# Performance work log

Hardware: AMD Instinct MI355X
Metric: run time of the kernel (lower is better)

## Reference

```python
import jax, jax.numpy as jnp
import numpy as np

B, W, N, K = 8, 16, 40, 10
DN = DL = 128
DE = 128
H = 4
NEG_SLOPE = 0.2


def _build_graph():
    # per-graph ring adjacency: i -> (i+d) % N for d=1..K, in dense_to_sparse order (src-major, dst ascending)
    src0, dst0 = [], []
    for i in range(N):
        ds = sorted(((i + d) % N) for d in range(1, K + 1))
        src0 += [i] * K
        dst0 += ds
    src0 = np.asarray(src0)
    dst0 = np.asarray(dst0)
    G = B * W
    Epg = N * K
    offs = np.arange(G)[:, None] * N
    node_adj = np.stack([(src0[None] + offs).reshape(-1), (dst0[None] + offs).reshape(-1)])
    # line graph: for each node, pair every incoming edge with every outgoing edge (torch repeat/tile order)
    a0, a1, fe = [], [], []
    for num in range(N):
        inc = np.nonzero(dst0 == num)[0]
        out = np.nonzero(src0 == num)[0]
        a0.append(np.repeat(inc, out.size))
        a1.append(np.tile(out, inc.size))
        fe.append(np.full(inc.size * out.size, num))
    a0, a1, fe = np.concatenate(a0), np.concatenate(a1), np.concatenate(fe)
    keep = a0 != a1  # remove_self_loops (no-op here, kept for fidelity)
    a0, a1, fe = a0[keep], a1[keep], fe[keep]
    eoffs = np.arange(G)[:, None] * Epg
    edge_adj = np.stack([(a0[None] + eoffs).reshape(-1), (a1[None] + eoffs).reshape(-1)])
    edge_efea = (fe[None] + offs).reshape(-1)
    return node_adj, edge_adj, edge_efea


def setup_inputs() -> dict:
    key = jax.random.key(0)
    node_adj, edge_adj, edge_efea = _build_graph()
    Epg = N * K
    D1 = DN + DL
    ks = jax.random.split(key, 16)

    def lin(k, fi, fo):
        return jax.random.normal(k, (fi, fo), jnp.float32) / np.sqrt(fi).astype(np.float32)

    return dict(
        x_node=jax.random.normal(ks[0], (B, W, N, DN), jnp.float32),
        x_trace=jax.random.normal(ks[1], (B, W, Epg, DE), jnp.float32),
        x_log=jax.random.normal(ks[2], (B, W, N, DL), jnp.float32),
        node_adj=jnp.asarray(node_adj, jnp.int32),
        edge_adj=jnp.asarray(edge_adj, jnp.int32),
        edge_efea=jnp.asarray(edge_efea, jnp.int32),
        Wl1=lin(ks[3], D1, D1), bl1=jnp.zeros((D1,), jnp.float32),
        Wr1=lin(ks[4], D1, D1), br1=jnp.zeros((D1,), jnp.float32),
        We1=lin(ks[5], DE, D1), be1=jnp.zeros((D1,), jnp.float32),
        att1=jax.random.normal(ks[6], (H, D1 // H), jnp.float32) / np.sqrt(D1 // H).astype(np.float32),
        bias1=jnp.zeros((D1,), jnp.float32),
        Wl2=lin(ks[7], DE, DE), bl2=jnp.zeros((DE,), jnp.float32),
        Wr2=lin(ks[8], DE, DE), br2=jnp.zeros((DE,), jnp.float32),
        We2=lin(ks[9], D1, DE), be2=jnp.zeros((DE,), jnp.float32),
        att2=jax.random.normal(ks[10], (H, DE // H), jnp.float32) / np.sqrt(DE // H).astype(np.float32),
        bias2=jnp.zeros((DE,), jnp.float32),
    )


def _gatv2(x, edge_index, edge_attr, Wl, bl, Wr, br, We, be, att, bias, heads):
    """PyG GATv2Conv (eval mode, add_self_loops=False, concat heads)."""
    n = x.shape[0]
    HC = Wl.shape[1]
    C = HC // heads
    xl = (x @ Wl + bl).reshape(n, heads, C)  # source transform
    xr = (x @ Wr + br).reshape(n, heads, C)  # target transform
    src, dst = edge_index[0], edge_index[1]
    ea = (edge_attr @ We + be).reshape(-1, heads, C)
    m = jax.nn.leaky_relu(xl[src] + xr[dst] + ea, NEG_SLOPE)  # [E,H,C]
    logits = jnp.einsum('ehc,hc->eh', m, att)
    # segment softmax over incoming edges per target node
    mx = jax.ops.segment_max(logits, dst, num_segments=n)
    mx = jnp.where(jnp.isfinite(mx), mx, 0.0)
    ex = jnp.exp(logits - mx[dst])
    den = jax.ops.segment_sum(ex, dst, num_segments=n)
    alpha = ex / (den[dst] + 1e-16)
    out = jax.ops.segment_sum(alpha[:, :, None] * xl[src], dst, num_segments=n)  # [n,H,C]
    return out.reshape(n, HC) + bias


def reference(x_node, x_trace, x_log, node_adj, edge_adj, edge_efea,
              Wl1, bl1, Wr1, br1, We1, be1, att1, bias1,
              Wl2, bl2, Wr2, br2, We2, be2, att2, bias2):
    b, w, n, dn = x_node.shape
    dl = x_log.shape[-1]
    node = jnp.concatenate([x_node, x_log], axis=-1).reshape(-1, dn + dl)  # [G*N, Dn+Dl]
    trace = x_trace.reshape(-1, x_trace.shape[-1])                          # [G*Epg, De]
    node = _gatv2(node, node_adj, trace, Wl1, bl1, Wr1, br1, We1, be1, att1, bias1, H)
    trace = _gatv2(trace, edge_adj, node[edge_efea], Wl2, bl2, Wr2, br2, We2, be2, att2, bias2, H)
    x_node_o = node[:, :dn].reshape(b, w, n, dn)
    x_trace_o = trace.reshape(b, w, -1, trace.shape[-1])
    x_log_o = node[:, dn:].reshape(b, w, n, dl)
    return (x_node_o, x_trace_o, x_log_o)
```

## Files before the change

### kernel.cpp

```cpp
#include <hip/hip_runtime.h>
#include <hip/hip_bf16.h>

#define D1 256
#define DE 128
#define KDEG 10
#define NPG 40
#define EPG 400
#define LOG2E 1.44269504088896340736f

typedef __attribute__((ext_vector_type(8))) short short8;
typedef __attribute__((ext_vector_type(4))) float f32x4;

static inline int cdiv(size_t a, int b) { return (int)((a + b - 1) / b); }
static inline size_t al256(size_t x) { return (x + 255) & ~(size_t)255; }

__device__ __forceinline__ short f2b(float x) {
  __hip_bfloat16 h = __float2bfloat16(x);
  return *reinterpret_cast<short*>(&h);
}

__device__ __forceinline__ short8 cvt8(const float* __restrict__ src) {
  float4 v0 = *(const float4*)src;
  float4 v1 = *(const float4*)(src + 4);
  short8 t;
  t[0] = f2b(v0.x); t[1] = f2b(v0.y); t[2] = f2b(v0.z); t[3] = f2b(v0.w);
  t[4] = f2b(v1.x); t[5] = f2b(v1.y); t[6] = f2b(v1.z); t[7] = f2b(v1.w);
  return t;
}

__global__ __launch_bounds__(256) void k_setup(const float* __restrict__ xn,
                                               const float* __restrict__ xlg,
                                               const float* __restrict__ xtr,
                                               const float* __restrict__ Wl1,
                                               const float* __restrict__ Wr1,
                                               const float* __restrict__ We1,
                                               const float* __restrict__ Wl2,
                                               const float* __restrict__ Wr2,
                                               const float* __restrict__ We2,
                                               const float* __restrict__ bl1,
                                               const float* __restrict__ br1,
                                               const float* __restrict__ be1,
                                               const float* __restrict__ bl2,
                                               const float* __restrict__ br2,
                                               float* __restrict__ den1,
                                               int* __restrict__ cnt,
                                               short* __restrict__ Xb,
                                               short* __restrict__ xtr_b,
                                               short* __restrict__ WT12,
                                               short* __restrict__ WTall,
                                               short* __restrict__ We2T,
                                               float* __restrict__ blr1,
                                               float* __restrict__ bfull,
                                               int NN, int NE) {
  size_t idx = (size_t)blockIdx.x * 256 + threadIdx.x;
  size_t n;
  n = (size_t)NN * 4;       if (idx < n) { den1[idx] = 0.f; return; }           idx -= n;
  n = (size_t)NN;           if (idx < n) { cnt[idx] = 0; return; }              idx -= n;
  n = (size_t)NN * 32;
  if (idx < n) {
    int row = (int)(idx >> 5), q = (int)(idx & 31);
    const float* src = (q < 16) ? &xn[(size_t)row * 128 + q * 8]
                                : &xlg[(size_t)row * 128 + (q - 16) * 8];
    *(short8*)&Xb[(size_t)row * 256 + q * 8] = cvt8(src);
    return;
  }
  idx -= n;
  n = (size_t)NE * 16;
  if (idx < n) {
    *(short8*)&xtr_b[idx * 8] = cvt8(&xtr[idx * 8]);
    return;
  }
  idx -= n;
  n = 512 * 256;
  if (idx < n) {
    int nn = (int)(idx >> 8), k = (int)(idx & 255);
    float v = (nn < 256) ? Wl1[(size_t)k * 256 + nn] : Wr1[(size_t)k * 256 + (nn - 256)];
    WT12[idx] = f2b(v);
    return;
  }
  idx -= n;
  n = 512 * 128;
  if (idx < n) {
    int nn = (int)(idx >> 7), k = (int)(idx & 127);
    float v;
    if (nn < 256)      v = We1[(size_t)k * 256 + nn];
    else if (nn < 384) v = Wl2[(size_t)k * 128 + (nn - 256)];
    else               v = Wr2[(size_t)k * 128 + (nn - 384)];
    WTall[idx] = f2b(v);
    return;
  }
  idx -= n;
  n = 128 * 256;
  if (idx < n) {
    int nn = (int)(idx >> 8), k = (int)(idx & 255);
    We2T[idx] = f2b(We2[(size_t)k * 128 + nn]);
    return;
  }
  idx -= n;
  n = 512;
  if (idx < n) { blr1[idx] = (idx < 256) ? bl1[idx] : br1[idx - 256]; return; }
  idx -= n;
  n = 512;
  if (idx < n) {
    bfull[idx] = (idx < 256) ? be1[idx] : (idx < 384 ? bl2[idx - 256] : br2[idx - 384]);
  }
}

__global__ __launch_bounds__(256) void k_build_inc(const int* __restrict__ adj,
                                                   int* __restrict__ cnt,
                                                   int* __restrict__ inc, int NE) {
  int e = blockIdx.x * 256 + threadIdx.x;
  if (e >= NE) return;
  int dst = adj[NE + e];
  int slot = atomicAdd(&cnt[dst], 1);
  inc[dst * KDEG + slot] = e;
}

__global__ __launch_bounds__(256) void k_gemm_mfma64(const short* __restrict__ A,
                                                     const short* __restrict__ WT,
                                                     const float* __restrict__ bias,
                                                     float* __restrict__ C,
                                                     int M, int K, int N) {
  __shared__ __align__(16) short As[64][40];
  __shared__ __align__(16) short Bs[64][40];
  const int tid = threadIdx.x;
  const int wave = tid >> 6, lane = tid & 63;
  const int quad = lane >> 4, l16 = lane & 15;
  const int m0 = blockIdx.y * 64, n0 = blockIdx.x * 64;
  const int wm = (wave & 1) * 32, wn = (wave >> 1) * 32;
  f32x4 acc[2][2] = {};
  for (int k0 = 0; k0 < K; k0 += 32) {
    {
      int r = tid >> 2, kc = (tid & 3) << 3;
      *(short8*)&As[r][kc] = *(const short8*)&A[(size_t)(m0 + r) * K + (k0 + kc)];
      *(short8*)&Bs[r][kc] = *(const short8*)&WT[(size_t)(n0 + r) * K + (k0 + kc)];
    }
    __syncthreads();
    short8 af[2], bf[2];
    #pragma unroll
    for (int mt = 0; mt < 2; ++mt)
      af[mt] = *(const short8*)&As[wm + mt * 16 + l16][quad << 3];
    #pragma unroll
    for (int nt = 0; nt < 2; ++nt)
      bf[nt] = *(const short8*)&Bs[wn + nt * 16 + l16][quad << 3];
    #pragma unroll
    for (int mt = 0; mt < 2; ++mt)
      #pragma unroll
      for (int nt = 0; nt < 2; ++nt)
        acc[mt][nt] = __builtin_amdgcn_mfma_f32_16x16x32_bf16(
            af[mt], bf[nt], acc[mt][nt], 0, 0, 0);
    __syncthreads();
  }
  #pragma unroll
  for (int nt = 0; nt < 2; ++nt) {
    int col = n0 + wn + nt * 16 + l16;
    float bs = bias[col];
    #pragma unroll
    for (int mt = 0; mt < 2; ++mt) {
      int row = m0 + wm + mt * 16 + (quad << 2);
      #pragma unroll
      for (int r = 0; r < 4; ++r)
        C[(size_t)(row + r) * N + col] = acc[mt][nt][r] + bs;
    }
  }
}

__global__ __launch_bounds__(256) void k_gemm_mega(const short* __restrict__ A,
                                                   const short* __restrict__ WT,
                                                   const float* __restrict__ bfull,
                                                   const float* __restrict__ att1,
                                                   const int* __restrict__ adj,
                                                   const float* __restrict__ xlr1,
                                                   float* __restrict__ logit1,
                                                   float* __restrict__ den1,
                                                   float* __restrict__ pool2,
                                                   int NE) {
  const int K = 128;
  struct SmemGemm { short As[128][40]; short Bs[128][40]; };
  struct SmemEpi  { int sdst[128]; float sxl[14][132]; float sxr[NPG][132]; };
  __shared__ __align__(16) union { SmemGemm g; SmemEpi e; } sm;
  const int tid = threadIdx.x;
  const int wave = tid >> 6, lane = tid & 63;
  const int quad = lane >> 4, l16 = lane & 15;
  int bid = blockIdx.x;
  int l = (bid & 7) * ((int)gridDim.x >> 3) + (bid >> 3);
  const int n0 = (l & 3) << 7;
  const int m0 = (l >> 2) << 7;
  const int wm = (wave & 1) * 64, wn = (wave >> 1) * 64;
  f32x4 acc[4][4] = {};
  for (int k0 = 0; k0 < K; k0 += 32) {
    #pragma unroll
    for (int s = 0; s < 2; ++s) {
      int ch = tid + s * 256;
      int r = ch >> 2, kc = (ch & 3) << 3;
      *(short8*)&sm.g.As[r][kc] = *(const short8*)&A[(size_t)(m0 + r) * K + (k0 + kc)];
      *(short8*)&sm.g.Bs[r][kc] = *(const short8*)&WT[(size_t)(n0 + r) * K + (k0 + kc)];
    }
    __syncthreads();
    short8 af[4], bf[4];
    #pragma unroll
    for (int mt = 0; mt < 4; ++mt)
      af[mt] = *(const short8*)&sm.g.As[wm + mt * 16 + l16][quad << 3];
    #pragma unroll
    for (int nt = 0; nt < 4; ++nt)
      bf[nt] = *(const short8*)&sm.g.Bs[wn + nt * 16 + l16][quad << 3];
    #pragma unroll
    for (int mt = 0; mt < 4; ++mt)
      #pragma unroll
      for (int nt = 0; nt < 4; ++nt)
        acc[mt][nt] = __builtin_amdgcn_mfma_f32_16x16x32_bf16(
            af[mt], bf[nt], acc[mt][nt], 0, 0, 0);
    __syncthreads();
  }
  if (n0 < 256) {
    const int gl = m0 / EPG;
    const int gh = (m0 + 127) / EPG;
    const int slo = m0 / KDEG;
    const int nrl = (m0 + 127) / KDEG - slo + 1;
    if (tid < 128) sm.e.sdst[tid] = adj[NE + m0 + tid];
    for (int s = tid; s < nrl * 128; s += 256) {
      int row = s >> 7, c = s & 127;
      sm.e.sxl[row][c] = xlr1[(size_t)(slo + row) * 512 + n0 + c];
    }
    const int h = (n0 + wn) >> 6;
    float attv[4], bev[4];
    int ccl[4];
    #pragma unroll
    for (int nt = 0; nt < 4; ++nt) {
      int col = n0 + wn + nt * 16 + l16;
      ccl[nt] = col - n0;
      attv[nt] = att1[col] * LOG2E;
      bev[nt] = bfull[col];
    }
    for (int g = gl; g <= gh; ++g) {
      __syncthreads();
      for (int s = tid; s < NPG * 128; s += 256) {
        int row = s >> 7, c = s & 127;
        sm.e.sxr[row][c] = xlr1[(size_t)(g * NPG + row) * 512 + 256 + n0 + c];
      }
      __syncthreads();
      const int elo = g * EPG, ehi = elo + EPG;
      #pragma unroll
      for (int mt = 0; mt < 4; ++mt) {
        #pragma unroll
        for (int r = 0; r < 4; ++r) {
          int le = wm + mt * 16 + (quad << 2) + r;
          int e = m0 + le;
          if (e < elo || e >= ehi) continue;
          int srow = e / KDEG - slo;
          int d = sm.e.sdst[le];
          int drow = d - g * NPG;
          float p = 0.f;
          #pragma unroll
          for (int nt = 0; nt < 4; ++nt) {
            float v = acc[mt][nt][r] + bev[nt] + sm.e.sxl[srow][ccl[nt]]
                    + sm.e.sxr[drow][ccl[nt]];
            v = (v > 0.f) ? v : 0.2f * v;
            p += v * attv[nt];
          }
          p += __shfl_xor(p, 1, 64);
          p += __shfl_xor(p, 2, 64);
          p += __shfl_xor(p, 4, 64);
          p += __shfl_xor(p, 8, 64);
          if (l16 == 0) {
            float ex = exp2f(p);
            logit1[(size_t)e * 4 + h] = ex;
            atomicAdd(&den1[(size_t)d * 4 + h], ex);
          }
        }
      }
    }
  } else {
    #pragma unroll
    for (int nt = 0; nt < 4; ++nt) {
      int col = n0 + wn + nt * 16 + l16;
      float bs = bfull[col];
      int pcol = col - 256;
      #pragma unroll
      for (int mt = 0; mt < 4; ++mt) {
        int row = m0 + wm + mt * 16 + (quad << 2);
        #pragma unroll
        for (int r = 0; r < 4; ++r)
          pool2[(size_t)(row + r) * 256 + pcol] = acc[mt][nt][r] + bs;
      }
    }
  }
}

__global__ __launch_bounds__(256) void k_agg1(const int* __restrict__ adj,
                                              const int* __restrict__ inc,
                                              const float* __restrict__ xlr1,
                                              const float* __restrict__ logit1,
                                              const float* __restrict__ den1,
                                              const float* __restrict__ bias1,
                                              short* __restrict__ nodeoutb,
                                              float* __restrict__ out_node,
                                              float* __restrict__ out_log) {
  int u = blockIdx.x, c = threadIdx.x;
  __shared__ int se[KDEG], ssrc[KDEG];
  __shared__ float slg[KDEG * 4];
  if (c < KDEG) se[c] = inc[u * KDEG + c];
  __syncthreads();
  if (c < KDEG) ssrc[c] = adj[se[c]];
  else if (c >= 64 && c < 64 + KDEG * 4) {
    int t = c - 64;
    slg[t] = logit1[(size_t)se[t >> 2] * 4 + (t & 3)];
  }
  __syncthreads();
  int h = c >> 6;
  float rden = 1.f / (den1[(size_t)u * 4 + h] + 1e-16f);
  float acc = 0.f;
  #pragma unroll
  for (int j = 0; j < KDEG; ++j)
    acc += slg[j * 4 + h] * xlr1[(size_t)ssrc[j] * 512 + c];
  float val = acc * rden + bias1[c];
  nodeoutb[(size_t)u * D1 + c] = f2b(val);
  if (c < 128) out_node[(size_t)u * 128 + c] = val;
  else         out_log[(size_t)u * 128 + (c - 128)] = val;
}

__global__ __launch_bounds__(256) void k_gat2_v4(const int* __restrict__ eadj,
                                                 const int* __restrict__ efea,
                                                 const float* __restrict__ pool2,
                                                 const float* __restrict__ nproj,
                                                 const float* __restrict__ att2,
                                                 const float* __restrict__ bias2,
                                                 float* __restrict__ out_trace,
                                                 int NL) {
  int gi = blockIdx.x;
  size_t le0 = (size_t)gi * 100;
  int t = threadIdx.x;
  __shared__ int ein[KDEG], eout[KDEG], nvs;
  __shared__ float xs[KDEG][132];
  __shared__ float rs[KDEG][132];
  __shared__ float as_[DE];
  __shared__ float exs[400];
  __shared__ float rdn[40];
  if (t < KDEG)          ein[t] = eadj[le0 + (size_t)t * KDEG];
  else if (t < 2 * KDEG) eout[t - KDEG] = eadj[(size_t)NL + le0 + (t - KDEG)];
  else if (t == 255)     nvs = efea[le0];
  __syncthreads();
  int nv = nvs;
  for (int s = t; s < 320; s += 256) {
    int j = s >> 5, q = (s & 31) << 2;
    *(float4*)&xs[j][q] = *(const float4*)&pool2[(size_t)ein[j] * 256 + q];
    float4 tr4 = *(const float4*)&pool2[(size_t)eout[j] * 256 + 128 + q];
    float4 ea4 = *(const float4*)&nproj[(size_t)nv * DE + q];
    float4 r;
    r.x = tr4.x + ea4.x; r.y = tr4.y + ea4.y;
    r.z = tr4.z + ea4.z; r.w = tr4.w + ea4.w;
    *(float4*)&rs[j][q] = r;
  }
  if (t < 32) {
    float4 a4 = *(const float4*)&att2[t << 2];
    float4 o;
    o.x = a4.x * LOG2E; o.y = a4.y * LOG2E;
    o.z = a4.z * LOG2E; o.w = a4.w * LOG2E;
    *(float4*)&as_[t << 2] = o;
  }
  __syncthreads();
  for (int s = t; s < 400; s += 256) {
    int h = s & 3;
    int j = s / 40;
    int o = (s - j * 40) >> 2;
    const float* xa = &xs[j][h << 5];
    const float* ra = &rs[o][h << 5];
    const float* aa = &as_[h << 5];
    float p = 0.f;
    #pragma unroll
    for (int i = 0; i < 32; i += 4) {
      float4 xv = *(const float4*)&xa[i];
      float4 rv = *(const float4*)&ra[i];
      float4 av = *(const float4*)&aa[i];
      float v;
      v = xv.x + rv.x; v = (v > 0.f) ? v : 0.2f * v; p += v * av.x;
      v = xv.y + rv.y; v = (v > 0.f) ? v : 0.2f * v; p += v * av.y;
      v = xv.z + rv.z; v = (v > 0.f) ? v : 0.2f * v; p += v * av.z;
      v = xv.w + rv.w; v = (v > 0.f) ? v : 0.2f * v; p += v * av.w;
    }
    exs[s] = exp2f(p);
  }
  __syncthreads();
  if (t < 40) {
    float d = 0.f;
    #pragma unroll
    for (int j = 0; j < KDEG; ++j) d += exs[(j * 10 + (t >> 2)) * 4 + (t & 3)];
    rdn[t] = 1.f / d;
  }
  __syncthreads();
  {
    int c = t & 127, h = c >> 5, oh = (t >> 7) * 5;
    float bsv = bias2[c];
    #pragma unroll
    for (int oo = 0; oo < 5; ++oo) {
      int o = oh + oo;
      float acc = 0.f;
      #pragma unroll
      for (int j = 0; j < KDEG; ++j)
        acc += exs[(j * 10 + o) * 4 + h] * xs[j][c];
      out_trace[(size_t)eout[o] * DE + c] = acc * rdn[o * 4 + h] + bsv;
    }
  }
}

extern "C" void kernel_launch(void* const* d_in, const int* in_sizes, int n_in,
                              void* d_out, int out_size, void* d_ws, size_t ws_size,
                              hipStream_t stream) {
  const float* x_node   = (const float*)d_in[0];
  const float* x_trace  = (const float*)d_in[1];
  const float* x_log    = (const float*)d_in[2];
  const int*   node_adj = (const int*)d_in[3];
  const int*   edge_adj = (const int*)d_in[4];
  const int*   edge_efea= (const int*)d_in[5];
  const float* Wl1 = (const float*)d_in[6];
  const float* bl1 = (const float*)d_in[7];
  const float* Wr1 = (const float*)d_in[8];
  const float* br1 = (const float*)d_in[9];
  const float* We1 = (const float*)d_in[10];
  const float* be1 = (const float*)d_in[11];
  const float* att1 = (const float*)d_in[12];
  const float* bias1 = (const float*)d_in[13];
  const float* Wl2 = (const float*)d_in[14];
  const float* bl2 = (const float*)d_in[15];
  const float* Wr2 = (const float*)d_in[16];
  const float* br2 = (const float*)d_in[17];
  const float* We2 = (const float*)d_in[18];
  const float* be2 = (const float*)d_in[19];
  const float* att2 = (const float*)d_in[20];
  const float* bias2 = (const float*)d_in[21];

  const int NN = in_sizes[0] / 128;
  const int NE = in_sizes[1] / 128;
  const int NL = in_sizes[5];

  char* p = (char*)d_ws;
  float* pool2   = (float*)p; p += al256((size_t)NE * 256 * 4);
  float* xlr1    = (float*)p; p += al256((size_t)NN * 512 * 4);
  short* Xb      = (short*)p; p += al256((size_t)NN * D1 * 2);
  short* xtr_b   = (short*)p; p += al256((size_t)NE * DE * 2);
  short* nodeoutb= (short*)p; p += al256((size_t)NN * D1 * 2);
  float* nproj   = (float*)p; p += al256((size_t)NN * DE * 4);
  float* logit1  = (float*)p; p += al256((size_t)NE * 4 * 4);
  float* den1    = (float*)p; p += al256((size_t)NN * 4 * 4);
  int*   inc     = (int*)p;   p += al256((size_t)NN * KDEG * 4);
  int*   cnt     = (int*)p;   p += al256((size_t)NN * 4);
  short* WT12    = (short*)p; p += al256((size_t)512 * 256 * 2);
  short* WTall   = (short*)p; p += al256((size_t)512 * 128 * 2);
  short* We2T    = (short*)p; p += al256((size_t)128 * 256 * 2);
  float* blr1    = (float*)p; p += al256(512 * 4);
  float* bfull   = (float*)p; p += al256(512 * 4);
  (void)ws_size;

  float* out_node  = (float*)d_out;
  float* out_trace = out_node + (size_t)NN * 128;
  float* out_log   = out_trace + (size_t)NE * 128;

  {
    size_t total = (size_t)NN * 5 + (size_t)NN * 32 + (size_t)NE * 16 +
                   512 * 256 + 512 * 128 + 128 * 256 + 512 + 512;
    k_setup<<<cdiv(total, 256), 256, 0, stream>>>(x_node, x_log, x_trace,
                                                  Wl1, Wr1, We1, Wl2, Wr2, We2,
                                                  bl1, br1, be1, bl2, br2,
                                                  den1, cnt, Xb, xtr_b,
                                                  WT12, WTall, We2T, blr1, bfull,
                                                  NN, NE);
  }
  k_build_inc<<<cdiv(NE, 256), 256, 0, stream>>>(node_adj, cnt, inc, NE);

  k_gemm_mfma64<<<dim3(512 / 64, NN / 64), 256, 0, stream>>>(Xb, WT12, blr1, xlr1,
                                                             NN, D1, 512);

  k_gemm_mega<<<4 * (NE / 128), 256, 0, stream>>>(xtr_b, WTall, bfull, att1,
                                                  node_adj, xlr1, logit1, den1,
                                                  pool2, NE);

  k_agg1<<<NN, 256, 0, stream>>>(node_adj, inc, xlr1, logit1, den1, bias1,
                                 nodeoutb, out_node, out_log);

  k_gemm_mfma64<<<dim3(DE / 64, NN / 64), 256, 0, stream>>>(nodeoutb, We2T, be2,
                                                            nproj, NN, D1, DE);
  k_gat2_v4<<<NN, 256, 0, stream>>>(edge_adj, edge_efea, pool2, nproj,
                                    att2, bias2, out_trace, NL);
}
```

Before: 236.9 us.

## Fuse layer-2 edge projections into GAT2 kernel, drop pool2 intermediate

```diff
diff --git a/kernel.cpp b/kernel.cpp
--- a/kernel.cpp
+++ b/kernel.cpp
@@ -6,6 +6,7 @@
 #define KDEG 10
 #define NPG 40
 #define EPG 400
+#define GNODES 2
 #define LOG2E 1.44269504088896340736f
 
 typedef __attribute__((ext_vector_type(8))) short short8;
@@ -173,7 +174,6 @@
                                                    const float* __restrict__ xlr1,
                                                    float* __restrict__ logit1,
                                                    float* __restrict__ den1,
-                                                   float* __restrict__ pool2,
                                                    int NE) {
   const int K = 128;
   struct SmemGemm { short As[128][40]; short Bs[128][40]; };
@@ -184,8 +184,8 @@
   const int quad = lane >> 4, l16 = lane & 15;
   int bid = blockIdx.x;
   int l = (bid & 7) * ((int)gridDim.x >> 3) + (bid >> 3);
-  const int n0 = (l & 3) << 7;
-  const int m0 = (l >> 2) << 7;
+  const int n0 = (l & 1) << 7;
+  const int m0 = (l >> 1) << 7;
   const int wm = (wave & 1) * 64, wn = (wave >> 1) * 64;
   f32x4 acc[4][4] = {};
   for (int k0 = 0; k0 < K; k0 += 32) {
@@ -212,76 +212,60 @@
             af[mt], bf[nt], acc[mt][nt], 0, 0, 0);
     __syncthreads();
   }
-  if (n0 < 256) {
-    const int gl = m0 / EPG;
-    const int gh = (m0 + 127) / EPG;
-    const int slo = m0 / KDEG;
-    const int nrl = (m0 + 127) / KDEG - slo + 1;
-    if (tid < 128) sm.e.sdst[tid] = adj[NE + m0 + tid];
-    for (int s = tid; s < nrl * 128; s += 256) {
+  const int gl = m0 / EPG;
+  const int gh = (m0 + 127) / EPG;
+  const int slo = m0 / KDEG;
+  const int nrl = (m0 + 127) / KDEG - slo + 1;
+  if (tid < 128) sm.e.sdst[tid] = adj[NE + m0 + tid];
+  for (int s = tid; s < nrl * 128; s += 256) {
+    int row = s >> 7, c = s & 127;
+    sm.e.sxl[row][c] = xlr1[(size_t)(slo + row) * 512 + n0 + c];
+  }
+  const int h = (n0 + wn) >> 6;
+  float attv[4], bev[4];
+  int ccl[4];
+  #pragma unroll
+  for (int nt = 0; nt < 4; ++nt) {
+    int col = n0 + wn + nt * 16 + l16;
+    ccl[nt] = col - n0;
+    attv[nt] = att1[col] * LOG2E;
+    bev[nt] = bfull[col];
+  }
+  for (int g = gl; g <= gh; ++g) {
+    __syncthreads();
+    for (int s = tid; s < NPG * 128; s += 256) {
       int row = s >> 7, c = s & 127;
-      sm.e.sxl[row][c] = xlr1[(size_t)(slo + row) * 512 + n0 + c];
-    }
-    const int h = (n0 + wn) >> 6;
-    float attv[4], bev[4];
-    int ccl[4];
-    #pragma unroll
-    for (int nt = 0; nt < 4; ++nt) {
-      int col = n0 + wn + nt * 16 + l16;
-      ccl[nt] = col - n0;
-      attv[nt] = att1[col] * LOG2E;
-      bev[nt] = bfull[col];
-    }
-    for (int g = gl; g <= gh; ++g) {
-      __syncthreads();
-      for (int s = tid; s < NPG * 128; s += 256) {
-        int row = s >> 7, c = s & 127;
-        sm.e.sxr[row][c] = xlr1[(size_t)(g * NPG + row) * 512 + 256 + n0 + c];
-      }
-      __syncthreads();
-      const int elo = g * EPG, ehi = elo + EPG;
-      #pragma unroll
-      for (int mt = 0; mt < 4; ++mt) {
+      sm.e.sxr[row][c] = xlr1[(size_t)(g * NPG + row) * 512 + 256 + n0 + c];
+    }
+    __syncthreads();
+    const int elo = g * EPG, ehi = elo + EPG;
+    #pragma unroll
+    for (int mt = 0; mt < 4; ++mt) {
+      #pragma unroll
+      for (int r = 0; r < 4; ++r) {
+        int le = wm + mt * 16 + (quad << 2) + r;
+        int e = m0 + le;
+        if (e < elo || e >= ehi) continue;
+        int srow = e / KDEG - slo;
+        int d = sm.e.sdst[le];
+        int drow = d - g * NPG;
+        float p = 0.f;
         #pragma unroll
-        for (int r = 0; r < 4; ++r) {
-          int le = wm + mt * 16 + (quad << 2) + r;
-          int e = m0 + le;
-          if (e < elo || e >= ehi) continue;
-          int srow = e / KDEG - slo;
-          int d = sm.e.sdst[le];
-          int drow = d - g * NPG;
-          float p = 0.f;
-          #pragma unroll
-          for (int nt = 0; nt < 4; ++nt) {
-            float v = acc[mt][nt][r] + bev[nt] + sm.e.sxl[srow][ccl[nt]]
-                    + sm.e.sxr[drow][ccl[nt]];
-            v = (v > 0.f) ? v : 0.2f * v;
-            p += v * attv[nt];
-          }
-          p += __shfl_xor(p, 1, 64);
-          p += __shfl_xor(p, 2, 64);
-          p += __shfl_xor(p, 4, 64);
-          p += __shfl_xor(p, 8, 64);
-          if (l16 == 0) {
-            float ex = exp2f(p);
-            logit1[(size_t)e * 4 + h] = ex;
-            atomicAdd(&den1[(size_t)d * 4 + h], ex);
-          }
+        for (int nt = 0; nt < 4; ++nt) {
+          float v = acc[mt][nt][r] + bev[nt] + sm.e.sxl[srow][ccl[nt]]
+                  + sm.e.sxr[drow][ccl[nt]];
+          v = (v > 0.f) ? v : 0.2f * v;
+          p += v * attv[nt];
         }
-      }
-    }
-  } else {
-    #pragma unroll
-    for (int nt = 0; nt < 4; ++nt) {
-      int col = n0 + wn + nt * 16 + l16;
-      float bs = bfull[col];
-      int pcol = col - 256;
-      #pragma unroll
-      for (int mt = 0; mt < 4; ++mt) {
-        int row = m0 + wm + mt * 16 + (quad << 2);
-        #pragma unroll
-        for (int r = 0; r < 4; ++r)
-          pool2[(size_t)(row + r) * 256 + pcol] = acc[mt][nt][r] + bs;
+        p += __shfl_xor(p, 1, 64);
+        p += __shfl_xor(p, 2, 64);
+        p += __shfl_xor(p, 4, 64);
+        p += __shfl_xor(p, 8, 64);
+        if (l16 == 0) {
+          float ex = exp2f(p);
+          logit1[(size_t)e * 4 + h] = ex;
+          atomicAdd(&den1[(size_t)d * 4 + h], ex);
+        }
       }
     }
   }
@@ -319,38 +303,41 @@
   else         out_log[(size_t)u * 128 + (c - 128)] = val;
 }
 
-__global__ __launch_bounds__(256) void k_gat2_v4(const int* __restrict__ eadj,
+__global__ __launch_bounds__(256) void k_gat2_v5(const int* __restrict__ eadj,
                                                  const int* __restrict__ efea,
-                                                 const float* __restrict__ pool2,
+                                                 const short* __restrict__ xtr_b,
+                                                 const short* __restrict__ WTall,
+                                                 const float* __restrict__ bl2,
+                                                 const float* __restrict__ br2,
                                                  const float* __restrict__ nproj,
                                                  const float* __restrict__ att2,
                                                  const float* __restrict__ bias2,
                                                  float* __restrict__ out_trace,
                                                  int NL) {
-  int gi = blockIdx.x;
-  size_t le0 = (size_t)gi * 100;
   int t = threadIdx.x;
+  const int wave = t >> 6, lane = t & 63;
+  const int quad = lane >> 4, l16 = lane & 15;
+  __shared__ __align__(16) short sA[32][136];
   __shared__ int ein[KDEG], eout[KDEG], nvs;
   __shared__ float xs[KDEG][132];
   __shared__ float rs[KDEG][132];
   __shared__ float as_[DE];
   __shared__ float exs[400];
   __shared__ float rdn[40];
-  if (t < KDEG)          ein[t] = eadj[le0 + (size_t)t * KDEG];
-  else if (t < 2 * KDEG) eout[t - KDEG] = eadj[(size_t)NL + le0 + (t - KDEG)];
-  else if (t == 255)     nvs = efea[le0];
-  __syncthreads();
-  int nv = nvs;
-  for (int s = t; s < 320; s += 256) {
-    int j = s >> 5, q = (s & 31) << 2;
-    *(float4*)&xs[j][q] = *(const float4*)&pool2[(size_t)ein[j] * 256 + q];
-    float4 tr4 = *(const float4*)&pool2[(size_t)eout[j] * 256 + 128 + q];
-    float4 ea4 = *(const float4*)&nproj[(size_t)nv * DE + q];
-    float4 r;
-    r.x = tr4.x + ea4.x; r.y = tr4.y + ea4.y;
-    r.z = tr4.z + ea4.z; r.w = tr4.w + ea4.w;
-    *(float4*)&rs[j][q] = r;
-  }
+  const int c0 = wave * 32 + l16;
+  short8 bfL[2][4], bfR[2][4];
+  #pragma unroll
+  for (int nt = 0; nt < 2; ++nt) {
+    int col = c0 + nt * 16;
+    #pragma unroll
+    for (int ks = 0; ks < 4; ++ks) {
+      bfL[nt][ks] = *(const short8*)&WTall[(size_t)(256 + col) * 128 + ks * 32 + (quad << 3)];
+      bfR[nt][ks] = *(const short8*)&WTall[(size_t)(384 + col) * 128 + ks * 32 + (quad << 3)];
+    }
+  }
+  float blv[2], brv[2];
+  blv[0] = bl2[c0]; blv[1] = bl2[c0 + 16];
+  brv[0] = br2[c0]; brv[1] = br2[c0 + 16];
   if (t < 32) {
     float4 a4 = *(const float4*)&att2[t << 2];
     float4 o;
@@ -358,47 +345,90 @@
     o.z = a4.z * LOG2E; o.w = a4.w * LOG2E;
     *(float4*)&as_[t << 2] = o;
   }
-  __syncthreads();
-  for (int s = t; s < 400; s += 256) {
-    int h = s & 3;
-    int j = s / 40;
-    int o = (s - j * 40) >> 2;
-    const float* xa = &xs[j][h << 5];
-    const float* ra = &rs[o][h << 5];
-    const float* aa = &as_[h << 5];
-    float p = 0.f;
-    #pragma unroll
-    for (int i = 0; i < 32; i += 4) {
-      float4 xv = *(const float4*)&xa[i];
-      float4 rv = *(const float4*)&ra[i];
-      float4 av = *(const float4*)&aa[i];
-      float v;
-      v = xv.x + rv.x; v = (v > 0.f) ? v : 0.2f * v; p += v * av.x;
-      v = xv.y + rv.y; v = (v > 0.f) ? v : 0.2f * v; p += v * av.y;
-      v = xv.z + rv.z; v = (v > 0.f) ? v : 0.2f * v; p += v * av.z;
-      v = xv.w + rv.w; v = (v > 0.f) ? v : 0.2f * v; p += v * av.w;
-    }
-    exs[s] = exp2f(p);
-  }
-  __syncthreads();
-  if (t < 40) {
-    float d = 0.f;
-    #pragma unroll
-    for (int j = 0; j < KDEG; ++j) d += exs[(j * 10 + (t >> 2)) * 4 + (t & 3)];
-    rdn[t] = 1.f / d;
-  }
-  __syncthreads();
-  {
-    int c = t & 127, h = c >> 5, oh = (t >> 7) * 5;
-    float bsv = bias2[c];
-    #pragma unroll
-    for (int oo = 0; oo < 5; ++oo) {
-      int o = oh + oo;
-      float acc = 0.f;
-      #pragma unroll
-      for (int j = 0; j < KDEG; ++j)
-        acc += exs[(j * 10 + o) * 4 + h] * xs[j][c];
-      out_trace[(size_t)eout[o] * DE + c] = acc * rdn[o * 4 + h] + bsv;
+  for (int ni = 0; ni < GNODES; ++ni) {
+    int gi = blockIdx.x * GNODES + ni;
+    size_t le0 = (size_t)gi * 100;
+    __syncthreads();
+    if (t < KDEG)            ein[t] = eadj[le0 + (size_t)t * KDEG];
+    else if (t < 2 * KDEG)   eout[t - KDEG] = eadj[(size_t)NL + le0 + (t - KDEG)];
+    else if (t == 255)       nvs = efea[le0];
+    __syncthreads();
+    for (int s = t; s < 320; s += 256) {
+      int slot = s >> 4, q = (s & 15) << 3;
+      int row = (slot < KDEG) ? slot : slot + 6;
+      int e = (slot < KDEG) ? ein[slot] : eout[slot - KDEG];
+      *(short8*)&sA[row][q] = *(const short8*)&xtr_b[(size_t)e * 128 + q];
+    }
+    int nv = nvs;
+    float npv0 = nproj[(size_t)nv * DE + c0];
+    float npv1 = nproj[(size_t)nv * DE + c0 + 16];
+    __syncthreads();
+    f32x4 accL[2] = {}, accR[2] = {};
+    #pragma unroll
+    for (int ks = 0; ks < 4; ++ks) {
+      short8 afL = *(const short8*)&sA[l16][ks * 32 + (quad << 3)];
+      short8 afR = *(const short8*)&sA[16 + l16][ks * 32 + (quad << 3)];
+      #pragma unroll
+      for (int nt = 0; nt < 2; ++nt) {
+        accL[nt] = __builtin_amdgcn_mfma_f32_16x16x32_bf16(afL, bfL[nt][ks], accL[nt], 0, 0, 0);
+        accR[nt] = __builtin_amdgcn_mfma_f32_16x16x32_bf16(afR, bfR[nt][ks], accR[nt], 0, 0, 0);
+      }
+    }
+    #pragma unroll
+    for (int nt = 0; nt < 2; ++nt) {
+      int col = c0 + nt * 16;
+      float np = nt ? npv1 : npv0;
+      #pragma unroll
+      for (int r = 0; r < 4; ++r) {
+        int j = (quad << 2) + r;
+        if (j < KDEG) {
+          xs[j][col] = accL[nt][r] + blv[nt];
+          rs[j][col] = accR[nt][r] + brv[nt] + np;
+        }
+      }
+    }
+    __syncthreads();
+    for (int s = t; s < 400; s += 256) {
+      int h = s & 3;
+      int j = s / 40;
+      int o = (s - j * 40) >> 2;
+      const float* xa = &xs[j][h << 5];
+      const float* ra = &rs[o][h << 5];
+      const float* aa = &as_[h << 5];
+      float p = 0.f;
+      #pragma unroll
+      for (int i = 0; i < 32; i += 4) {
+        float4 xv = *(const float4*)&xa[i];
+        float4 rv = *(const float4*)&ra[i];
+        float4 av = *(const float4*)&aa[i];
+        float v;
+        v = xv.x + rv.x; v = (v > 0.f) ? v : 0.2f * v; p += v * av.x;
+        v = xv.y + rv.y; v = (v > 0.f) ? v : 0.2f * v; p += v * av.y;
+        v = xv.z + rv.z; v = (v > 0.f) ? v : 0.2f * v; p += v * av.z;
+        v = xv.w + rv.w; v = (v > 0.f) ? v : 0.2f * v; p += v * av.w;
+      }
+      exs[s] = exp2f(p);
+    }
+    __syncthreads();
+    if (t < 40) {
+      float d = 0.f;
+      #pragma unroll
+      for (int j = 0; j < KDEG; ++j) d += exs[(j * 10 + (t >> 2)) * 4 + (t & 3)];
+      rdn[t] = 1.f / d;
+    }
+    __syncthreads();
+    {
+      int c = t & 127, h = c >> 5, oh = (t >> 7) * 5;
+      float bsv = bias2[c];
+      #pragma unroll
+      for (int oo = 0; oo < 5; ++oo) {
+        int o = oh + oo;
+        float acc = 0.f;
+        #pragma unroll
+        for (int j = 0; j < KDEG; ++j)
+          acc += exs[(j * 10 + o) * 4 + h] * xs[j][c];
+        out_trace[(size_t)eout[o] * DE + c] = acc * rdn[o * 4 + h] + bsv;
+      }
     }
   }
 }
@@ -434,7 +464,6 @@
   const int NL = in_sizes[5];
 
   char* p = (char*)d_ws;
-  float* pool2   = (float*)p; p += al256((size_t)NE * 256 * 4);
   float* xlr1    = (float*)p; p += al256((size_t)NN * 512 * 4);
   short* Xb      = (short*)p; p += al256((size_t)NN * D1 * 2);
   short* xtr_b   = (short*)p; p += al256((size_t)NE * DE * 2);
@@ -470,15 +499,16 @@
   k_gemm_mfma64<<<dim3(512 / 64, NN / 64), 256, 0, stream>>>(Xb, WT12, blr1, xlr1,
                                                              NN, D1, 512);
 
-  k_gemm_mega<<<4 * (NE / 128), 256, 0, stream>>>(xtr_b, WTall, bfull, att1,
+  k_gemm_mega<<<2 * (NE / 128), 256, 0, stream>>>(xtr_b, WTall, bfull, att1,
                                                   node_adj, xlr1, logit1, den1,
-                                                  pool2, NE);
+                                                  NE);
 
   k_agg1<<<NN, 256, 0, stream>>>(node_adj, inc, xlr1, logit1, den1, bias1,
                                  nodeoutb, out_node, out_log);
 
   k_gemm_mfma64<<<dim3(DE / 64, NN / 64), 256, 0, stream>>>(nodeoutb, We2T, be2,
                                                             nproj, NN, D1, DE);
-  k_gat2_v4<<<NN, 256, 0, stream>>>(edge_adj, edge_efea, pool2, nproj,
-                                    att2, bias2, out_trace, NL);
-}
+  k_gat2_v5<<<NN / GNODES, 256, 0, stream>>>(edge_adj, edge_efea, xtr_b, WTall,
+                                             bl2, br2, nproj, att2, bias2,
+                                             out_trace, NL);
+}
```

After: 260.8 us. 10.1% more time.

## Drop atomic softmax denominators; recompute per node in agg1, reshape gat2 logits per wave

Applied to the files above, without the earlier changes.

```diff
diff --git a/kernel.cpp b/kernel.cpp
--- a/kernel.cpp
+++ b/kernel.cpp
@@ -42,7 +42,6 @@
                                                const float* __restrict__ be1,
                                                const float* __restrict__ bl2,
                                                const float* __restrict__ br2,
-                                               float* __restrict__ den1,
                                                int* __restrict__ cnt,
                                                short* __restrict__ Xb,
                                                short* __restrict__ xtr_b,
@@ -54,7 +53,6 @@
                                                int NN, int NE) {
   size_t idx = (size_t)blockIdx.x * 256 + threadIdx.x;
   size_t n;
-  n = (size_t)NN * 4;       if (idx < n) { den1[idx] = 0.f; return; }           idx -= n;
   n = (size_t)NN;           if (idx < n) { cnt[idx] = 0; return; }              idx -= n;
   n = (size_t)NN * 32;
   if (idx < n) {
@@ -172,7 +170,6 @@
                                                    const int* __restrict__ adj,
                                                    const float* __restrict__ xlr1,
                                                    float* __restrict__ logit1,
-                                                   float* __restrict__ den1,
                                                    float* __restrict__ pool2,
                                                    int NE) {
   const int K = 128;
@@ -263,9 +260,7 @@
           p += __shfl_xor(p, 4, 64);
           p += __shfl_xor(p, 8, 64);
           if (l16 == 0) {
-            float ex = exp2f(p);
-            logit1[(size_t)e * 4 + h] = ex;
-            atomicAdd(&den1[(size_t)d * 4 + h], ex);
+            logit1[(size_t)e * 4 + h] = exp2f(p);
           }
         }
       }
@@ -291,7 +286,6 @@
                                               const int* __restrict__ inc,
                                               const float* __restrict__ xlr1,
                                               const float* __restrict__ logit1,
-                                              const float* __restrict__ den1,
                                               const float* __restrict__ bias1,
                                               short* __restrict__ nodeoutb,
                                               float* __restrict__ out_node,
@@ -308,7 +302,10 @@
   }
   __syncthreads();
   int h = c >> 6;
-  float rden = 1.f / (den1[(size_t)u * 4 + h] + 1e-16f);
+  float den = 0.f;
+  #pragma unroll
+  for (int j = 0; j < KDEG; ++j) den += slg[j * 4 + h];
+  float rden = 1.f / (den + 1e-16f);
   float acc = 0.f;
   #pragma unroll
   for (int j = 0; j < KDEG; ++j)
@@ -330,6 +327,7 @@
   int gi = blockIdx.x;
   size_t le0 = (size_t)gi * 100;
   int t = threadIdx.x;
+  const int wave = t >> 6, lane = t & 63;
   __shared__ int ein[KDEG], eout[KDEG], nvs;
   __shared__ float xs[KDEG][132];
   __shared__ float rs[KDEG][132];
@@ -359,26 +357,28 @@
     *(float4*)&as_[t << 2] = o;
   }
   __syncthreads();
-  for (int s = t; s < 400; s += 256) {
-    int h = s & 3;
-    int j = s / 40;
-    int o = (s - j * 40) >> 2;
-    const float* xa = &xs[j][h << 5];
-    const float* ra = &rs[o][h << 5];
+  {
+    int h = wave;
     const float* aa = &as_[h << 5];
-    float p = 0.f;
-    #pragma unroll
-    for (int i = 0; i < 32; i += 4) {
-      float4 xv = *(const float4*)&xa[i];
-      float4 rv = *(const float4*)&ra[i];
-      float4 av = *(const float4*)&aa[i];
-      float v;
-      v = xv.x + rv.x; v = (v > 0.f) ? v : 0.2f * v; p += v * av.x;
-      v = xv.y + rv.y; v = (v > 0.f) ? v : 0.2f * v; p += v * av.y;
-      v = xv.z + rv.z; v = (v > 0.f) ? v : 0.2f * v; p += v * av.z;
-      v = xv.w + rv.w; v = (v > 0.f) ? v : 0.2f * v; p += v * av.w;
-    }
-    exs[s] = exp2f(p);
+    for (int idx = lane; idx < 100; idx += 64) {
+      int j = idx / 10;
+      int o = idx - j * 10;
+      const float* xa = &xs[j][h << 5];
+      const float* ra = &rs[o][h << 5];
+      float p = 0.f;
+      #pragma unroll
+      for (int i = 0; i < 32; i += 4) {
+        float4 xv = *(const float4*)&xa[i];
+        float4 rv = *(const float4*)&ra[i];
+        float4 av = *(const float4*)&aa[i];
+        float v;
+        v = xv.x + rv.x; v = (v > 0.f) ? v : 0.2f * v; p += v * av.x;
+        v = xv.y + rv.y; v = (v > 0.f) ? v : 0.2f * v; p += v * av.y;
+        v = xv.z + rv.z; v = (v > 0.f) ? v : 0.2f * v; p += v * av.z;
+        v = xv.w + rv.w; v = (v > 0.f) ? v : 0.2f * v; p += v * av.w;
+      }
+      exs[(j * 10 + o) * 4 + h] = exp2f(p);
+    }
   }
   __syncthreads();
   if (t < 40) {
@@ -441,7 +441,6 @@
   short* nodeoutb= (short*)p; p += al256((size_t)NN * D1 * 2);
   float* nproj   = (float*)p; p += al256((size_t)NN * DE * 4);
   float* logit1  = (float*)p; p += al256((size_t)NE * 4 * 4);
-  float* den1    = (float*)p; p += al256((size_t)NN * 4 * 4);
   int*   inc     = (int*)p;   p += al256((size_t)NN * KDEG * 4);
   int*   cnt     = (int*)p;   p += al256((size_t)NN * 4);
   short* WT12    = (short*)p; p += al256((size_t)512 * 256 * 2);
@@ -456,12 +455,12 @@
   float* out_log   = out_trace + (size_t)NE * 128;
 
   {
-    size_t total = (size_t)NN * 5 + (size_t)NN * 32 + (size_t)NE * 16 +
+    size_t total = (size_t)NN + (size_t)NN * 32 + (size_t)NE * 16 +
                    512 * 256 + 512 * 128 + 128 * 256 + 512 + 512;
     k_setup<<<cdiv(total, 256), 256, 0, stream>>>(x_node, x_log, x_trace,
                                                   Wl1, Wr1, We1, Wl2, Wr2, We2,
                                                   bl1, br1, be1, bl2, br2,
-                                                  den1, cnt, Xb, xtr_b,
+                                                  cnt, Xb, xtr_b,
                                                   WT12, WTall, We2T, blr1, bfull,
                                                   NN, NE);
   }
@@ -471,10 +470,10 @@
                                                              NN, D1, 512);
 
   k_gemm_mega<<<4 * (NE / 128), 256, 0, stream>>>(xtr_b, WTall, bfull, att1,
-                                                  node_adj, xlr1, logit1, den1,
+                                                  node_adj, xlr1, logit1,
                                                   pool2, NE);
 
-  k_agg1<<<NN, 256, 0, stream>>>(node_adj, inc, xlr1, logit1, den1, bias1,
+  k_agg1<<<NN, 256, 0, stream>>>(node_adj, inc, xlr1, logit1, bias1,
                                  nodeoutb, out_node, out_log);
 
   k_gemm_mfma64<<<dim3(DE / 64, NN / 64), 256, 0, stream>>>(nodeoutb, We2T, be2,
```

Result: faster. 231.6 us (-2.3%).
